# Performance work log

Measured on AMD Instinct MI355X. Metric: run time of the kernel, lower is better.

## Reference

```python
import jax, jax.numpy as jnp
import numpy as np

D_MODEL = 1024
NHEAD = 16
HEAD_DIM = D_MODEL // NHEAD
HIDDEN = 4 * D_MODEL  # SwiGLU hidden_dim
B, L = 2, 2048
EPS = 1e-8


def _alibi_slopes(n):
    # standard ALiBi slopes: geometric sequence 2^(-8/n * i)
    return np.array([2 ** (-8.0 / n * (i + 1)) for i in range(n)], dtype=np.float32)


def setup_inputs() -> dict:
    key = jax.random.key(0)
    ks = jax.random.split(key, 10)
    x = jax.random.normal(ks[0], (B, L, D_MODEL), dtype=jnp.float32)
    # causal mask: True where attention is disallowed (j > i)
    attn_mask = jnp.triu(jnp.ones((L, L), dtype=bool), k=1)[None, None]
    # ALiBi bias: -slope * (i - j) for j <= i; value on masked positions irrelevant
    pos = jnp.arange(L)
    dist = (pos[:, None] - pos[None, :]).astype(jnp.float32)  # [L,L]
    slopes = jnp.asarray(_alibi_slopes(NHEAD))
    alibi_bias = (-slopes[:, None, None] * dist)[None]  # [1,H,L,L]
    s = 0.02
    w_qkv = jax.random.normal(ks[1], (D_MODEL, 3 * D_MODEL), dtype=jnp.float32) * s
    b_qkv = jnp.zeros((3 * D_MODEL,), jnp.float32)
    w_o = jax.random.normal(ks[2], (D_MODEL, D_MODEL), dtype=jnp.float32) * s
    b_o = jnp.zeros((D_MODEL,), jnp.float32)
    scale1 = jnp.ones((D_MODEL,), jnp.float32)
    scale2 = jnp.ones((D_MODEL,), jnp.float32)
    w1 = jax.random.normal(ks[3], (D_MODEL, 2 * HIDDEN), dtype=jnp.float32) * s
    b1 = jnp.zeros((2 * HIDDEN,), jnp.float32)
    w2 = jax.random.normal(ks[4], (HIDDEN, D_MODEL), dtype=jnp.float32) * s
    b2 = jnp.zeros((D_MODEL,), jnp.float32)
    return dict(x=x, attn_mask=attn_mask, alibi_bias=alibi_bias,
                w_qkv=w_qkv, b_qkv=b_qkv, w_o=w_o, b_o=b_o,
                scale1=scale1, scale2=scale2, w1=w1, b1=b1, w2=w2, b2=b2)


def rmsnorm(x, scale):
    return scale * (x * jax.lax.rsqrt(jnp.mean(x * x, axis=-1, keepdims=True) + EPS))


def reference(x, attn_mask, alibi_bias, w_qkv, b_qkv, w_o, b_o,
              scale1, scale2, w1, b1, w2, b2):
    Bv, Lv, D = x.shape
    xn = rmsnorm(x, scale1)
    qkv = xn @ w_qkv + b_qkv  # [B,L,3D]
    q, k, v = jnp.split(qkv, 3, axis=-1)
    def to_heads(t):
        return t.reshape(Bv, Lv, NHEAD, HEAD_DIM).transpose(0, 2, 1, 3)  # [B,H,L,Dh]
    q, k, v = to_heads(q), to_heads(k), to_heads(v)
    scores = jnp.einsum('bhqd,bhkd->bhqk', q, k) / (HEAD_DIM ** 0.5)
    scores = scores + alibi_bias[:, :, :Lv, :Lv]
    scores = jnp.where(attn_mask, -jnp.inf, scores)
    attn = jax.nn.softmax(scores, axis=-1)
    out = jnp.einsum('bhqk,bhkd->bhqd', attn, v)  # [B,H,L,Dh]
    out = out.transpose(0, 2, 1, 3).reshape(Bv, Lv, D)
    x = x + (out @ w_o + b_o)
    # SwiGLU FFN
    h = rmsnorm(x, scale2) @ w1 + b1
    x_proj, gate = jnp.split(h, 2, axis=-1)
    ffn = (jax.nn.silu(gate) * x_proj) @ w2 + b2
    return x + ffn
```

## Files before the change

kernel.cpp:

```cpp
#include <hip/hip_runtime.h>
#include <hip/hip_bf16.h>
#include <stdint.h>

typedef __hip_bfloat16 bf16;
typedef __bf16 bf16x8 __attribute__((ext_vector_type(8)));
typedef float f32x4 __attribute__((ext_vector_type(4)));

#define DM   1024
#define LSEQ 2048
#define NH   16
#define DH   64
#define BB   2
#define HID  4096
#define MROWS (BB*LSEQ)
#define QLD  (3*DM)

__device__ __forceinline__ void load_lds16(const void* g, void* l) {
    __builtin_amdgcn_global_load_lds(
        (const __attribute__((address_space(1))) unsigned int*)g,
        (__attribute__((address_space(3))) unsigned int*)l, 16, 0, 0);
}

__global__ __launch_bounds__(256)
void transpose_all(const float* __restrict__ wqkv, const float* __restrict__ wo,
                   const float* __restrict__ w1, const float* __restrict__ w2,
                   bf16* __restrict__ wqkvT, bf16* __restrict__ woT,
                   bf16* __restrict__ w1T, bf16* __restrict__ w2T) {
    int bid = blockIdx.x;
    const float* src; bf16* dst; int R, C, bx, by; bool inter = false;
    if (bid < 3072)       { src = wqkv; dst = wqkvT; R = 1024; C = 3072; bx = bid % 96;  by = bid / 96; }
    else if (bid < 4096)  { bid -= 3072;  src = wo; dst = woT;  R = 1024; C = 1024; bx = bid % 32;  by = bid / 32; }
    else if (bid < 12288) { bid -= 4096;  src = w1; dst = w1T;  R = 1024; C = 8192; bx = bid % 256; by = bid / 256; inter = true; }
    else                  { bid -= 12288; src = w2; dst = w2T;  R = 4096; C = 1024; bx = bid % 32;  by = bid / 32; }
    __shared__ float tile[32][33];
    const int c0 = bx * 32, r0 = by * 32;
    const int tx = threadIdx.x & 31, ty = threadIdx.x >> 5;
#pragma unroll
    for (int i = 0; i < 32; i += 8)
        tile[ty + i][tx] = src[(size_t)(r0 + ty + i) * C + c0 + tx];
    __syncthreads();
#pragma unroll
    for (int i = 0; i < 32; i += 8) {
        const int c = c0 + ty + i;
        const int drow = inter ? ((c < HID) ? 2 * c : 2 * (c - HID) + 1) : c;
        dst[(size_t)drow * R + r0 + tx] = __float2bfloat16(tile[tx][ty + i]);
    }
}

__global__ __launch_bounds__(256)
void v_transpose(const bf16* __restrict__ qkv, bf16* __restrict__ vt) {
    const int bh = blockIdx.z, b = bh >> 4, h = bh & 15;
    const int l0 = blockIdx.x * 32, d0 = blockIdx.y * 32;
    __shared__ bf16 tile[32][33];
    const int tx = threadIdx.x & 31, ty = threadIdx.x >> 5;
#pragma unroll
    for (int i = 0; i < 32; i += 8)
        tile[ty + i][tx] = qkv[((size_t)b * LSEQ + l0 + ty + i) * QLD + 2 * DM + h * DH + d0 + tx];
    __syncthreads();
#pragma unroll
    for (int i = 0; i < 32; i += 8)
        vt[((size_t)bh * DH + d0 + ty + i) * LSEQ + l0 + tx] = tile[tx][ty + i];
}

__global__ __launch_bounds__(256)
void rmsnorm_cast(const float* __restrict__ x, const float* __restrict__ scale,
                  bf16* __restrict__ out) {
    const int row = blockIdx.x;
    const int tid = threadIdx.x;
    const float4 v = ((const float4*)(x + (size_t)row * DM))[tid];
    float ss = v.x * v.x + v.y * v.y + v.z * v.z + v.w * v.w;
#pragma unroll
    for (int off = 32; off >= 1; off >>= 1) ss += __shfl_xor(ss, off);
    __shared__ float part[4];
    if ((tid & 63) == 0) part[tid >> 6] = ss;
    __syncthreads();
    const float tot = part[0] + part[1] + part[2] + part[3];
    const float rs = rsqrtf(tot * (1.0f / DM) + 1e-8f);
    const float4 s = ((const float4*)scale)[tid];
    union { bf16 h[4]; uint2 u; } pk;
    pk.h[0] = __float2bfloat16(v.x * rs * s.x);
    pk.h[1] = __float2bfloat16(v.y * rs * s.y);
    pk.h[2] = __float2bfloat16(v.z * rs * s.z);
    pk.h[3] = __float2bfloat16(v.w * rs * s.w);
    ((uint2*)(out + (size_t)row * DM))[tid] = pk.u;
}

template <int KDIM, int NN, typename Epi>
__global__ __launch_bounds__(256, 3)
void gemm_bt(const bf16* __restrict__ A, const bf16* __restrict__ Bt, Epi epi) {
    __shared__ __align__(16) bf16 sA[3][128 * 32];
    __shared__ __align__(16) bf16 sB[3][128 * 32];
    constexpr int NPX = NN / 8;
    const int bid = blockIdx.x;
    const int xcd = bid & 7, loc = bid >> 3;
    const int nb = xcd * NPX + (loc % NPX), mb = loc / NPX;
    const int m0 = mb * 128, n0 = nb * 128;
    const int tid = threadIdx.x;
    const int wave = tid >> 6, lane = tid & 63;
    const int lo = lane & 15, hi = lane >> 4;
    const int wm = wave & 1, wn = wave >> 1;
    const int rowA = lane >> 2, cc = (lane & 3) * 8;
    const int slot0 = wave * 2, slot1 = wave * 2 + 1;

    const bf16* Ag0 = A + (size_t)(m0 + slot0 * 16 + rowA) * KDIM + cc;
    const bf16* Ag1 = A + (size_t)(m0 + slot1 * 16 + rowA) * KDIM + cc;
    const bf16* Bg0 = Bt + (size_t)(n0 + slot0 * 16 + rowA) * KDIM + cc;
    const bf16* Bg1 = Bt + (size_t)(n0 + slot1 * 16 + rowA) * KDIM + cc;

    auto stage = [&](int kt, int buf) {
        const int k0 = kt * 32;
        load_lds16(Ag0 + k0, &sA[buf][slot0 * 512]);
        load_lds16(Ag1 + k0, &sA[buf][slot1 * 512]);
        load_lds16(Bg0 + k0, &sB[buf][slot0 * 512]);
        load_lds16(Bg1 + k0, &sB[buf][slot1 * 512]);
    };

    f32x4 acc[4][4];
#pragma unroll
    for (int i = 0; i < 4; i++)
#pragma unroll
        for (int j = 0; j < 4; j++) acc[i][j] = (f32x4){0.f, 0.f, 0.f, 0.f};

    constexpr int NK = KDIM / 32;
    stage(0, 0);
    int bc = 0;
    for (int kt = 0; kt < NK; ++kt) {
        const int bn = (bc == 2) ? 0 : bc + 1;
        if (kt + 1 < NK) {
            stage(kt + 1, bn);
            asm volatile("s_waitcnt vmcnt(4)" ::: "memory");
        } else {
            asm volatile("s_waitcnt vmcnt(0)" ::: "memory");
        }
        asm volatile("s_barrier" ::: "memory");
        const bf16* cA = sA[bc];
        const bf16* cB = sB[bc];
        bf16x8 a[4], b[4];
#pragma unroll
        for (int i = 0; i < 4; i++)
            a[i] = *(const bf16x8*)&cA[(wm * 64 + i * 16 + lo) * 32 + hi * 8];
#pragma unroll
        for (int j = 0; j < 4; j++)
            b[j] = *(const bf16x8*)&cB[(wn * 64 + j * 16 + lo) * 32 + hi * 8];
#pragma unroll
        for (int i = 0; i < 4; i++)
#pragma unroll
            for (int j = 0; j < 4; j++)
                acc[i][j] = __builtin_amdgcn_mfma_f32_16x16x32_bf16(a[i], b[j], acc[i][j], 0, 0, 0);
        bc = bn;
    }
#pragma unroll
    for (int i = 0; i < 4; i++) {
        const int row = m0 + wm * 64 + i * 16 + hi * 4;
#pragma unroll
        for (int j = 0; j < 4; j++) {
            const int col = n0 + wn * 64 + j * 16 + lo;
#pragma unroll
            for (int r = 0; r < 4; r++) epi(row + r, col, acc[i][j][r]);
        }
    }
}

struct EpiBiasBF16 {
    const float* bias; bf16* out; int ldc;
    __device__ void operator()(int row, int col, float val) const {
        out[(size_t)row * ldc + col] = __float2bfloat16(val + bias[col]);
    }
};
struct EpiBiasResidF32 {
    const float* bias; const float* res; float* out; int ldc;
    __device__ void operator()(int row, int col, float val) const {
        const size_t idx = (size_t)row * ldc + col;
        out[idx] = val + bias[col] + res[idx];
    }
};
struct EpiSwiGLU {
    const float* b1; bf16* out;
    __device__ void operator()(int row, int col, float val) const {
        const int orig = (col >> 1) + ((col & 1) ? HID : 0);
        const float v = val + b1[orig];
        const float other = __shfl_xor(v, 1);
        const float g = other;
        const float s = g / (1.f + __expf(-g));
        if (!(threadIdx.x & 1))
            out[(size_t)row * HID + (col >> 1)] = __float2bfloat16(s * v);
    }
};

__global__ __launch_bounds__(256, 2)
void attn_flash(const bf16* __restrict__ qkv, const bf16* __restrict__ Vt,
                bf16* __restrict__ O) {
    const int bh = blockIdx.x;
    const int qt = gridDim.y - 1 - blockIdx.y;
    const int b = bh >> 4, h = bh & 15;
    const int tid = threadIdx.x, wave = tid >> 6, lane = tid & 63;
    const int lo = lane & 15, hi = lane >> 4;
    __shared__ __align__(16) bf16 sQ[64 * 64];
    __shared__ __align__(16) bf16 sK[3][64 * 64];
    __shared__ __align__(16) bf16 sV[3][64 * 64];
    __shared__ __align__(16) bf16 sP[4][16 * 64];

    const float LOG2E = 1.44269504088896340736f;
    const float slope2 = exp2f(-0.5f * (float)(h + 1)) * LOG2E;
    const float qscale = 0.125f * LOG2E;
    const float SHIFT = 34.0f;
    const int q0 = qt * 64;
    const bf16* Qb = qkv + (size_t)b * LSEQ * QLD + h * DH;
    const bf16* Kb = Qb + DM;
    const bf16* Vb = Vt + (size_t)bh * DH * LSEQ;

    const int s0 = wave * 2, s1 = wave * 2 + 1;
    auto stageKV = [&](int kt, int buf) {
        load_lds16(Kb + (size_t)(kt * 64 + s0 * 8 + (lane >> 3)) * QLD + (lane & 7) * 8, &sK[buf][s0 * 512]);
        load_lds16(Kb + (size_t)(kt * 64 + s1 * 8 + (lane >> 3)) * QLD + (lane & 7) * 8, &sK[buf][s1 * 512]);
        load_lds16(Vb + (size_t)(s0 * 8 + (lane >> 3)) * LSEQ + kt * 64 + (lane & 7) * 8, &sV[buf][s0 * 512]);
        load_lds16(Vb + (size_t)(s1 * 8 + (lane >> 3)) * LSEQ + kt * 64 + (lane & 7) * 8, &sV[buf][s1 * 512]);
    };

#pragma unroll
    for (int i = 0; i < 2; ++i) {
        const int s = wave * 2 + i;
        load_lds16(Qb + (size_t)(q0 + s * 8 + (lane >> 3)) * QLD + (lane & 7) * 8, &sQ[s * 512]);
    }
    __syncthreads();
    bf16x8 aq0 = *(const bf16x8*)&sQ[(wave * 16 + lo) * 64 + hi * 8];
    bf16x8 aq1 = *(const bf16x8*)&sQ[(wave * 16 + lo) * 64 + 32 + hi * 8];

    bf16x8 vone;
#pragma unroll
    for (int t = 0; t < 8; t++) vone[t] = (__bf16)1.0f;

    f32x4 accO[4];
#pragma unroll
    for (int j = 0; j < 4; j++) accO[j] = (f32x4){0.f, 0.f, 0.f, 0.f};
    f32x4 accL = (f32x4){0.f, 0.f, 0.f, 0.f};
    const int irow0 = q0 + wave * 16 + hi * 4;

    stageKV(0, 0);
    int bc = 0;
    for (int kt = 0; kt <= qt; ++kt) {
        const int bn = (bc == 2) ? 0 : bc + 1;
        if (kt < qt) {
            stageKV(kt + 1, bn);
            asm volatile("s_waitcnt vmcnt(4)" ::: "memory");
        } else {
            asm volatile("s_waitcnt vmcnt(0)" ::: "memory");
        }
        asm volatile("s_barrier" ::: "memory");

#pragma unroll
        for (int j = 0; j < 4; j++) {
            bf16x8 bk0 = *(const bf16x8*)&sK[bc][(j * 16 + lo) * 64 + hi * 8];
            bf16x8 bk1 = *(const bf16x8*)&sK[bc][(j * 16 + lo) * 64 + 32 + hi * 8];
            f32x4 z = (f32x4){0.f, 0.f, 0.f, 0.f};
            z = __builtin_amdgcn_mfma_f32_16x16x32_bf16(aq0, bk0, z, 0, 0, 0);
            z = __builtin_amdgcn_mfma_f32_16x16x32_bf16(aq1, bk1, z, 0, 0, 0);
            const int jg = kt * 64 + j * 16 + lo;
#pragma unroll
            for (int r = 0; r < 4; r++) {
                const int ig = irow0 + r;
                const float pv = (jg > ig) ? 0.f
                    : exp2f(z[r] * qscale - slope2 * (float)(ig - jg) - SHIFT);
                sP[wave][(hi * 4 + r) * 64 + j * 16 + lo] = __float2bfloat16(pv);
            }
        }
        bf16x8 ap0 = *(const bf16x8*)&sP[wave][lo * 64 + hi * 8];
        bf16x8 ap1 = *(const bf16x8*)&sP[wave][lo * 64 + 32 + hi * 8];
        accL = __builtin_amdgcn_mfma_f32_16x16x32_bf16(ap0, vone, accL, 0, 0, 0);
        accL = __builtin_amdgcn_mfma_f32_16x16x32_bf16(ap1, vone, accL, 0, 0, 0);
#pragma unroll
        for (int j = 0; j < 4; j++) {
            bf16x8 bv0 = *(const bf16x8*)&sV[bc][(j * 16 + lo) * 64 + hi * 8];
            bf16x8 bv1 = *(const bf16x8*)&sV[bc][(j * 16 + lo) * 64 + 32 + hi * 8];
            accO[j] = __builtin_amdgcn_mfma_f32_16x16x32_bf16(ap0, bv0, accO[j], 0, 0, 0);
            accO[j] = __builtin_amdgcn_mfma_f32_16x16x32_bf16(ap1, bv1, accO[j], 0, 0, 0);
        }
        bc = bn;
    }
    bf16* Ob = O + (size_t)b * LSEQ * DM + (size_t)h * DH;
#pragma unroll
    for (int r = 0; r < 4; r++) {
        const float inv = 1.0f / accL[r];
        const int row = q0 + wave * 16 + hi * 4 + r;
#pragma unroll
        for (int j = 0; j < 4; j++)
            Ob[(size_t)row * DM + j * 16 + lo] = __float2bfloat16(accO[j][r] * inv);
    }
}

extern "C" void kernel_launch(void* const* d_in, const int* in_sizes, int n_in,
                              void* d_out, int out_size, void* d_ws, size_t ws_size,
                              hipStream_t stream) {
    const float* x      = (const float*)d_in[0];
    const float* w_qkv  = (const float*)d_in[3];
    const float* b_qkv  = (const float*)d_in[4];
    const float* w_o    = (const float*)d_in[5];
    const float* b_o    = (const float*)d_in[6];
    const float* scale1 = (const float*)d_in[7];
    const float* scale2 = (const float*)d_in[8];
    const float* w1     = (const float*)d_in[9];
    const float* b1     = (const float*)d_in[10];
    const float* w2     = (const float*)d_in[11];
    const float* b2     = (const float*)d_in[12];
    float* out = (float*)d_out;

    uint8_t* w = (uint8_t*)d_ws;
    size_t off = 0;
    auto take = [&](size_t bytes) { void* p = w + off; off += (bytes + 255) & ~(size_t)255; return p; };
    bf16* xn    = (bf16*)take((size_t)MROWS * DM * 2);
    bf16* wqkvT = (bf16*)take((size_t)3 * DM * DM * 2);
    bf16* woT   = (bf16*)take((size_t)DM * DM * 2);
    bf16* w1T   = (bf16*)take((size_t)2 * HID * DM * 2);
    bf16* w2T   = (bf16*)take((size_t)DM * HID * 2);
    bf16* qkvb  = (bf16*)take((size_t)MROWS * QLD * 2);
    bf16* vt    = (bf16*)take((size_t)MROWS * DM * 2);
    bf16* ao    = (bf16*)take((size_t)MROWS * DM * 2);
    float* x1   = (float*)take((size_t)MROWS * DM * 4);
    bf16* xn2   = (bf16*)take((size_t)MROWS * DM * 2);
    bf16* ffn   = (bf16*)take((size_t)MROWS * HID * 2);

    transpose_all<<<16384, 256, 0, stream>>>(w_qkv, w_o, w1, w2, wqkvT, woT, w1T, w2T);
    rmsnorm_cast<<<MROWS, 256, 0, stream>>>(x, scale1, xn);

    EpiBiasBF16 e1{b_qkv, qkvb, QLD};
    gemm_bt<DM, 24, EpiBiasBF16><<<32 * 24, 256, 0, stream>>>(xn, wqkvT, e1);

    v_transpose<<<dim3(LSEQ / 32, DH / 32, BB * NH), 256, 0, stream>>>(qkvb, vt);
    attn_flash<<<dim3(BB * NH, LSEQ / 64), 256, 0, stream>>>(qkvb, vt, ao);

    EpiBiasResidF32 e2{b_o, x, x1, DM};
    gemm_bt<DM, 8, EpiBiasResidF32><<<32 * 8, 256, 0, stream>>>(ao, woT, e2);

    rmsnorm_cast<<<MROWS, 256, 0, stream>>>(x1, scale2, xn2);

    EpiSwiGLU e3{b1, ffn};
    gemm_bt<DM, 64, EpiSwiGLU><<<32 * 64, 256, 0, stream>>>(xn2, w1T, e3);

    EpiBiasResidF32 e4{b2, x1, out, DM};
    gemm_bt<HID, 8, EpiBiasResidF32><<<32 * 8, 256, 0, stream>>>(ffn, w2T, e4);
}
```

Baseline: 698.4 us.

## Split-K the O-proj and FFN2 GEMMs, fuse reduce with RMSNorm, simplify ALiBi

```diff
diff --git a/kernel.cpp b/kernel.cpp
--- a/kernel.cpp
+++ b/kernel.cpp
@@ -85,14 +85,68 @@
     ((uint2*)(out + (size_t)row * DM))[tid] = pk.u;
 }
 
-template <int KDIM, int NN, typename Epi>
+__global__ __launch_bounds__(256)
+void oproj_reduce_rmsnorm(const float* __restrict__ part, const float* __restrict__ bias,
+                          const float* __restrict__ res, const float* __restrict__ scale,
+                          float* __restrict__ x1, bf16* __restrict__ xn2) {
+    const int row = blockIdx.x, tid = threadIdx.x;
+    const float4 p0 = ((const float4*)(part + (size_t)row * DM))[tid];
+    const float4 p1 = ((const float4*)(part + ((size_t)MROWS + row) * DM))[tid];
+    const float4 p2 = ((const float4*)(part + ((size_t)2 * MROWS + row) * DM))[tid];
+    const float4 bb = ((const float4*)bias)[tid];
+    const float4 rr = ((const float4*)(res + (size_t)row * DM))[tid];
+    float4 v;
+    v.x = p0.x + p1.x + p2.x + bb.x + rr.x;
+    v.y = p0.y + p1.y + p2.y + bb.y + rr.y;
+    v.z = p0.z + p1.z + p2.z + bb.z + rr.z;
+    v.w = p0.w + p1.w + p2.w + bb.w + rr.w;
+    ((float4*)(x1 + (size_t)row * DM))[tid] = v;
+    float ss = v.x * v.x + v.y * v.y + v.z * v.z + v.w * v.w;
+#pragma unroll
+    for (int off = 32; off >= 1; off >>= 1) ss += __shfl_xor(ss, off);
+    __shared__ float partl[4];
+    if ((tid & 63) == 0) partl[tid >> 6] = ss;
+    __syncthreads();
+    const float tot = partl[0] + partl[1] + partl[2] + partl[3];
+    const float rs = rsqrtf(tot * (1.0f / DM) + 1e-8f);
+    const float4 s = ((const float4*)scale)[tid];
+    union { bf16 h[4]; uint2 u; } pk;
+    pk.h[0] = __float2bfloat16(v.x * rs * s.x);
+    pk.h[1] = __float2bfloat16(v.y * rs * s.y);
+    pk.h[2] = __float2bfloat16(v.z * rs * s.z);
+    pk.h[3] = __float2bfloat16(v.w * rs * s.w);
+    ((uint2*)(xn2 + (size_t)row * DM))[tid] = pk.u;
+}
+
+__global__ __launch_bounds__(256)
+void ffn2_reduce(const float* __restrict__ part, const float* __restrict__ b2,
+                 const float* __restrict__ x1, float* __restrict__ out) {
+    const int g = blockIdx.x * 256 + threadIdx.x;
+    const int c4 = g & 255;
+    const float4 p0 = ((const float4*)part)[g];
+    const float4 p1 = ((const float4*)part)[(size_t)MROWS * 256 + g];
+    const float4 p2 = ((const float4*)part)[(size_t)2 * MROWS * 256 + g];
+    const float4 bb = ((const float4*)b2)[c4];
+    const float4 rr = ((const float4*)x1)[g];
+    float4 v;
+    v.x = p0.x + p1.x + p2.x + bb.x + rr.x;
+    v.y = p0.y + p1.y + p2.y + bb.y + rr.y;
+    v.z = p0.z + p1.z + p2.z + bb.z + rr.z;
+    v.w = p0.w + p1.w + p2.w + bb.w + rr.w;
+    ((float4*)out)[g] = v;
+}
+
+template <int KDIM, int NN, int S, typename Epi>
 __global__ __launch_bounds__(256, 3)
 void gemm_bt(const bf16* __restrict__ A, const bf16* __restrict__ Bt, Epi epi) {
     __shared__ __align__(16) bf16 sA[3][128 * 32];
     __shared__ __align__(16) bf16 sB[3][128 * 32];
     constexpr int NPX = NN / 8;
+    constexpr int MBNB = (MROWS / 128) * NN;
     const int bid = blockIdx.x;
-    const int xcd = bid & 7, loc = bid >> 3;
+    const int sk = (S > 1) ? bid / MBNB : 0;
+    const int ib = (S > 1) ? bid % MBNB : bid;
+    const int xcd = ib & 7, loc = ib >> 3;
     const int nb = xcd * NPX + (loc % NPX), mb = loc / NPX;
     const int m0 = mb * 128, n0 = nb * 128;
     const int tid = threadIdx.x;
@@ -122,11 +176,13 @@
         for (int j = 0; j < 4; j++) acc[i][j] = (f32x4){0.f, 0.f, 0.f, 0.f};
 
     constexpr int NK = KDIM / 32;
-    stage(0, 0);
+    const int kt0 = (S > 1) ? (sk * NK) / S : 0;
+    const int kt1 = (S > 1) ? ((sk + 1) * NK) / S : NK;
+    stage(kt0, 0);
     int bc = 0;
-    for (int kt = 0; kt < NK; ++kt) {
+    for (int kt = kt0; kt < kt1; ++kt) {
         const int bn = (bc == 2) ? 0 : bc + 1;
-        if (kt + 1 < NK) {
+        if (kt + 1 < kt1) {
             stage(kt + 1, bn);
             asm volatile("s_waitcnt vmcnt(4)" ::: "memory");
         } else {
@@ -149,9 +205,10 @@
                 acc[i][j] = __builtin_amdgcn_mfma_f32_16x16x32_bf16(a[i], b[j], acc[i][j], 0, 0, 0);
         bc = bn;
     }
+    const int rbase = sk * MROWS + m0;
 #pragma unroll
     for (int i = 0; i < 4; i++) {
-        const int row = m0 + wm * 64 + i * 16 + hi * 4;
+        const int row = rbase + wm * 64 + i * 16 + hi * 4;
 #pragma unroll
         for (int j = 0; j < 4; j++) {
             const int col = n0 + wn * 64 + j * 16 + lo;
@@ -167,11 +224,10 @@
         out[(size_t)row * ldc + col] = __float2bfloat16(val + bias[col]);
     }
 };
-struct EpiBiasResidF32 {
-    const float* bias; const float* res; float* out; int ldc;
+struct EpiStoreF32 {
+    float* out;
     __device__ void operator()(int row, int col, float val) const {
-        const size_t idx = (size_t)row * ldc + col;
-        out[idx] = val + bias[col] + res[idx];
+        out[(size_t)row * DM + col] = val;
     }
 };
 struct EpiSwiGLU {
@@ -236,6 +292,12 @@
     f32x4 accL = (f32x4){0.f, 0.f, 0.f, 0.f};
     const int irow0 = q0 + wave * 16 + hi * 4;
 
+    float cbase[4];
+#pragma unroll
+    for (int r = 0; r < 4; r++) cbase[r] = slope2 * (float)(lo - (irow0 + r)) - SHIFT;
+    const float jadd1 = slope2 * 16.f;
+    const float kadd = slope2 * 64.f;
+
     stageKV(0, 0);
     int bc = 0;
     for (int kt = 0; kt <= qt; ++kt) {
@@ -248,6 +310,7 @@
         }
         asm volatile("s_barrier" ::: "memory");
 
+        const bool diag = (kt == qt);
 #pragma unroll
         for (int j = 0; j < 4; j++) {
             bf16x8 bk0 = *(const bf16x8*)&sK[bc][(j * 16 + lo) * 64 + hi * 8];
@@ -255,15 +318,25 @@
             f32x4 z = (f32x4){0.f, 0.f, 0.f, 0.f};
             z = __builtin_amdgcn_mfma_f32_16x16x32_bf16(aq0, bk0, z, 0, 0, 0);
             z = __builtin_amdgcn_mfma_f32_16x16x32_bf16(aq1, bk1, z, 0, 0, 0);
-            const int jg = kt * 64 + j * 16 + lo;
-#pragma unroll
-            for (int r = 0; r < 4; r++) {
-                const int ig = irow0 + r;
-                const float pv = (jg > ig) ? 0.f
-                    : exp2f(z[r] * qscale - slope2 * (float)(ig - jg) - SHIFT);
-                sP[wave][(hi * 4 + r) * 64 + j * 16 + lo] = __float2bfloat16(pv);
+            const float cj = (float)j * jadd1;
+            if (diag) {
+                const int jg = kt * 64 + j * 16 + lo;
+#pragma unroll
+                for (int r = 0; r < 4; r++) {
+                    const float pv = (jg > irow0 + r) ? 0.f
+                        : exp2f(fmaf(z[r], qscale, cbase[r] + cj));
+                    sP[wave][(hi * 4 + r) * 64 + j * 16 + lo] = __float2bfloat16(pv);
+                }
+            } else {
+#pragma unroll
+                for (int r = 0; r < 4; r++) {
+                    const float pv = exp2f(fmaf(z[r], qscale, cbase[r] + cj));
+                    sP[wave][(hi * 4 + r) * 64 + j * 16 + lo] = __float2bfloat16(pv);
+                }
             }
         }
+#pragma unroll
+        for (int r = 0; r < 4; r++) cbase[r] += kadd;
         bf16x8 ap0 = *(const bf16x8*)&sP[wave][lo * 64 + hi * 8];
         bf16x8 ap1 = *(const bf16x8*)&sP[wave][lo * 64 + 32 + hi * 8];
         accL = __builtin_amdgcn_mfma_f32_16x16x32_bf16(ap0, vone, accL, 0, 0, 0);
@@ -318,24 +391,26 @@
     float* x1   = (float*)take((size_t)MROWS * DM * 4);
     bf16* xn2   = (bf16*)take((size_t)MROWS * DM * 2);
     bf16* ffn   = (bf16*)take((size_t)MROWS * HID * 2);
+    float* part1 = (float*)take((size_t)3 * MROWS * DM * 4);
+    float* part2 = (float*)take((size_t)3 * MROWS * DM * 4);
 
     transpose_all<<<16384, 256, 0, stream>>>(w_qkv, w_o, w1, w2, wqkvT, woT, w1T, w2T);
     rmsnorm_cast<<<MROWS, 256, 0, stream>>>(x, scale1, xn);
 
     EpiBiasBF16 e1{b_qkv, qkvb, QLD};
-    gemm_bt<DM, 24, EpiBiasBF16><<<32 * 24, 256, 0, stream>>>(xn, wqkvT, e1);
+    gemm_bt<DM, 24, 1, EpiBiasBF16><<<32 * 24, 256, 0, stream>>>(xn, wqkvT, e1);
 
     v_transpose<<<dim3(LSEQ / 32, DH / 32, BB * NH), 256, 0, stream>>>(qkvb, vt);
     attn_flash<<<dim3(BB * NH, LSEQ / 64), 256, 0, stream>>>(qkvb, vt, ao);
 
-    EpiBiasResidF32 e2{b_o, x, x1, DM};
-    gemm_bt<DM, 8, EpiBiasResidF32><<<32 * 8, 256, 0, stream>>>(ao, woT, e2);
-
-    rmsnorm_cast<<<MROWS, 256, 0, stream>>>(x1, scale2, xn2);
+    EpiStoreF32 e2{part1};
+    gemm_bt<DM, 8, 3, EpiStoreF32><<<3 * 32 * 8, 256, 0, stream>>>(ao, woT, e2);
+    oproj_reduce_rmsnorm<<<MROWS, 256, 0, stream>>>(part1, b_o, x, scale2, x1, xn2);
 
     EpiSwiGLU e3{b1, ffn};
-    gemm_bt<DM, 64, EpiSwiGLU><<<32 * 64, 256, 0, stream>>>(xn2, w1T, e3);
-
-    EpiBiasResidF32 e4{b2, x1, out, DM};
-    gemm_bt<HID, 8, EpiBiasResidF32><<<32 * 8, 256, 0, stream>>>(ffn, w2T, e4);
-}
+    gemm_bt<DM, 64, 1, EpiSwiGLU><<<32 * 64, 256, 0, stream>>>(xn2, w1T, e3);
+
+    EpiStoreF32 e4{part2};
+    gemm_bt<HID, 8, 3, EpiStoreF32><<<3 * 32 * 8, 256, 0, stream>>>(ffn, w2T, e4);
+    ffn2_reduce<<<MROWS, 256, 0, stream>>>(part2, b2, x1, out);
+}
```

Result: faster. 681.9 us (-2.4%).
